# Optimization experiments

Hardware: AMD Instinct MI355X
Metric: run time of the kernel (lower is better)

The kernel has to match this reference:

```python
import jax, jax.numpy as jnp
import numpy as np

D = 512; H = 8; DH = D // H; FFN = 2048; K = 31; N = 4; T = 1024


def _ln(x, g, b):
    m = jnp.mean(x, -1, keepdims=True)
    v = jnp.var(x, -1, keepdims=True)
    return (x - m) * jax.lax.rsqrt(v + 1e-5) * g + b


def _ff(x, g, b, w1, b1, w2, b2):
    h = jax.nn.silu(_ln(x, g, b) @ w1 + b1)
    return 0.5 * (h @ w2 + b2)


def _forward(x, rel_pe, ln1_g, ln1_b, ff1_w1, ff1_b1, ff1_w2, ff1_b2,
             an_g, an_b, wq, bq, wk, bk, wv, bv, wo, bo, pos_w, u, v,
             cn_g, cn_b, pe_w, pe_b, dw_w, dw_b, bn_g, bn_b, pc_w, pc_b,
             ln2_g, ln2_b, ff2_w1, ff2_b1, ff2_w2, ff2_b2, fn_g, fn_b):
    Nb, Tt, _ = x.shape
    # macaron FF 1 (half-step)
    x = x + _ff(x, ln1_g, ln1_b, ff1_w1, ff1_b1, ff1_w2, ff1_b2)

    # RPE multi-head attention (Transformer-XL style)
    xa = _ln(x, an_g, an_b)
    split = lambda m: m.reshape(Nb, Tt, H, DH).transpose(0, 2, 1, 3)  # (N,H,T,dh)
    Q = split(xa @ wq + bq)
    Kk = split(xa @ wk + bk)
    V = split(xa @ wv + bv)
    # content-to-content: (Q+u) K^T
    AC = jnp.einsum('nhtd,nhsd->nhts', Q + u[None, :, None, :], Kk)
    # content-to-position: (Q+v) R^T, then rel-shift gather
    R = (rel_pe @ pos_w).reshape(2 * Tt - 1, H, DH)  # (2T-1,H,dh)
    BD_raw = jnp.einsum('nhtd,phd->nhtp', Q + v[None, :, None, :], R)  # (N,H,T,2T-1)
    idx = jnp.arange(Tt - 1, -1, -1)[None, :] + jnp.arange(Tt)[:, None]  # (T,T): i-j+(T-1)
    BD = jnp.take_along_axis(BD_raw, idx[None, None, :, :], axis=-1)  # (N,H,T,T)
    scores = (AC + BD) * (DH ** -0.5)
    attn = jax.nn.softmax(scores, axis=-1)
    out = jnp.einsum('nhts,nhsd->nthd', attn, V).reshape(Nb, Tt, D)
    x = x + (out @ wo + bo)

    # conv module: LN -> pointwise expand -> GLU -> depthwise conv -> BN(eval) -> SiLU -> pointwise
    c = _ln(x, cn_g, cn_b) @ pe_w + pe_b  # (N,T,2D)
    a, g = jnp.split(c, 2, axis=-1)
    c = a * jax.nn.sigmoid(g)
    c = c.transpose(0, 2, 1)  # (N,D,T)
    c = jax.lax.conv_general_dilated(
        c, dw_w, window_strides=(1,), padding=[(K // 2, K // 2)],
        dimension_numbers=('NCH', 'OIH', 'NCH'), feature_group_count=D)
    c = c + dw_b[None, :, None]
    # BatchNorm1d in eval mode: running_mean=0, running_var=1
    c = c * bn_g[None, :, None] + bn_b[None, :, None]
    c = jax.nn.silu(c).transpose(0, 2, 1) @ pc_w + pc_b
    x = x + c

    # macaron FF 2 + final LN
    x = x + _ff(x, ln2_g, ln2_b, ff2_w1, ff2_b1, ff2_w2, ff2_b2)
    return _ln(x, fn_g, fn_b)


def setup_inputs() -> dict:
    keys = iter(jax.random.split(jax.random.key(0), 64))
    def rn(*shape, s=0.02):
        return jax.random.normal(next(keys), shape, jnp.float32) * s
    inp = {}
    inp['x'] = rn(N, T, D, s=1.0)
    inp['rel_pe'] = rn(2 * T - 1, D, s=1.0)
    inp['ln1_g'] = jnp.ones(D); inp['ln1_b'] = jnp.zeros(D)
    inp['ff1_w1'] = rn(D, FFN); inp['ff1_b1'] = jnp.zeros(FFN)
    inp['ff1_w2'] = rn(FFN, D); inp['ff1_b2'] = jnp.zeros(D)
    inp['an_g'] = jnp.ones(D); inp['an_b'] = jnp.zeros(D)
    inp['wq'] = rn(D, D); inp['bq'] = jnp.zeros(D)
    inp['wk'] = rn(D, D); inp['bk'] = jnp.zeros(D)
    inp['wv'] = rn(D, D); inp['bv'] = jnp.zeros(D)
    inp['wo'] = rn(D, D); inp['bo'] = jnp.zeros(D)
    inp['pos_w'] = rn(D, D)
    inp['u'] = rn(H, DH); inp['v'] = rn(H, DH)
    inp['cn_g'] = jnp.ones(D); inp['cn_b'] = jnp.zeros(D)
    inp['pe_w'] = rn(D, 2 * D); inp['pe_b'] = jnp.zeros(2 * D)
    inp['dw_w'] = rn(D, 1, K); inp['dw_b'] = jnp.zeros(D)
    inp['bn_g'] = jnp.ones(D); inp['bn_b'] = jnp.zeros(D)
    inp['pc_w'] = rn(D, D); inp['pc_b'] = jnp.zeros(D)
    inp['ln2_g'] = jnp.ones(D); inp['ln2_b'] = jnp.zeros(D)
    inp['ff2_w1'] = rn(D, FFN); inp['ff2_b1'] = jnp.zeros(FFN)
    inp['ff2_w2'] = rn(FFN, D); inp['ff2_b2'] = jnp.zeros(D)
    inp['fn_g'] = jnp.ones(D); inp['fn_b'] = jnp.zeros(D)
    return inp


def reference(x, rel_pe, ln1_g, ln1_b, ff1_w1, ff1_b1, ff1_w2, ff1_b2,
              an_g, an_b, wq, bq, wk, bk, wv, bv, wo, bo, pos_w, u, v,
              cn_g, cn_b, pe_w, pe_b, dw_w, dw_b, bn_g, bn_b, pc_w, pc_b,
              ln2_g, ln2_b, ff2_w1, ff2_b1, ff2_w2, ff2_b2, fn_g, fn_b):
    return _forward(x, rel_pe, ln1_g, ln1_b, ff1_w1, ff1_b1, ff1_w2, ff1_b2,
                    an_g, an_b, wq, bq, wk, bk, wv, bv, wo, bo, pos_w, u, v,
                    cn_g, cn_b, pe_w, pe_b, dw_w, dw_b, bn_g, bn_b, pc_w, pc_b,
                    ln2_g, ln2_b, ff2_w1, ff2_b1, ff2_w2, ff2_b2, fn_g, fn_b)
```

## Files before the change

### kernel.cpp

```cpp
#include <hip/hip_runtime.h>
#include <hip/hip_bf16.h>

using bf16 = __hip_bfloat16;
typedef __attribute__((ext_vector_type(8))) short short8;
typedef __attribute__((ext_vector_type(4))) float f32x4;

static __device__ __forceinline__ float b2f(bf16 v) { return __bfloat162float(v); }
static __device__ __forceinline__ bf16  f2b(float v) { return __float2bfloat16(v); }
static __device__ __forceinline__ short f2bs(float x) {
    union { float f; unsigned u; } c; c.f = x;
    unsigned r = (c.u + 0x7FFFu + ((c.u >> 16) & 1u)) >> 16;
    return (short)r;
}
static __device__ __forceinline__ float bs2f(short s) {
    union { unsigned u; float f; } c; c.u = ((unsigned)(unsigned short)s) << 16;
    return c.f;
}
static __device__ __forceinline__ void gload16(const short* g, short* l) {
    __builtin_amdgcn_global_load_lds(
        (const __attribute__((address_space(1))) void*)g,
        (__attribute__((address_space(3))) void*)l, 16, 0, 0);
}

constexpr int kD   = 512;
constexpr int kT   = 1024;
constexpr int kN   = 4;
constexpr int kH   = 8;
constexpr int kDH  = 64;
constexpr int kFFN = 2048;
constexpr int kROWS = kN * kT;
constexpr int kP    = 2 * kT - 1;

#define ACT_NONE 0
#define ACT_SILU 1

__global__ __launch_bounds__(256) void stamp_kernel(float* __restrict__ out, int n, float val) {
    int i = blockIdx.x * 256 + threadIdx.x;
    if (i < n) out[i] = (i == 0 ? val : 0.f);
}

__global__ __launch_bounds__(256) void cvt_kernel(const float* __restrict__ in,
                                                  float* __restrict__ out, int n4) {
    int i = blockIdx.x * 256 + threadIdx.x;
    if (i < n4) ((f32x4*)out)[i] = ((const f32x4*)in)[i];
}

struct WtDesc { const float* src; short* dst; int K; int N; int tstart; };
struct WtArgs { WtDesc d[11]; };

__global__ __launch_bounds__(256) void wt_all_kernel(WtArgs a) {
    __shared__ float t[32][33];
    int bid = blockIdx.x;
    int i = 0;
#pragma unroll
    for (int j = 1; j < 11; ++j) if (bid >= a.d[j].tstart) i = j;
    const float* W = a.d[i].src;
    short* Wt = a.d[i].dst;
    int Kd = a.d[i].K, Nd = a.d[i].N;
    int lt = bid - a.d[i].tstart;
    int nx = Nd >> 5;
    int n0 = (lt % nx) * 32, k0 = (lt / nx) * 32;
    int tx = threadIdx.x & 31, ty = threadIdx.x >> 5;
#pragma unroll
    for (int it = 0; it < 4; ++it)
        t[ty + it * 8][tx] = W[(size_t)(k0 + ty + it * 8) * Nd + n0 + tx];
    __syncthreads();
#pragma unroll
    for (int it = 0; it < 4; ++it)
        Wt[(size_t)(n0 + ty + it * 8) * Kd + k0 + tx] = f2bs(t[tx][ty + it * 8]);
}

__global__ __launch_bounds__(256) void vtrans_kernel(const bf16* __restrict__ V,
                                                     bf16* __restrict__ Vt) {
    __shared__ short ts[64][72];
    int tt = blockIdx.x, h = blockIdx.y, n = blockIdx.z;
    int tid = threadIdx.x;
    int r = tid >> 3, cg = (tid & 7) * 8;
#pragma unroll
    for (int it = 0; it < 2; ++it) {
        int row = it * 32 + r;
        *(short8*)&ts[row][cg] =
            *(const short8*)((const short*)V + ((size_t)n * kT + tt * 64 + row) * 512 + h * 64 + cg);
    }
    __syncthreads();
#pragma unroll
    for (int it = 0; it < 2; ++it) {
        int d = it * 32 + r;
        short8 o;
#pragma unroll
        for (int i = 0; i < 8; ++i) o[i] = ts[cg + i][d];
        *(short8*)((short*)Vt + ((size_t)(n * 8 + h) * 64 + d) * 1024 + tt * 64 + cg) = o;
    }
}

__global__ __launch_bounds__(256) void dwt_kernel(const float* __restrict__ dw_w,
                                                  const float* __restrict__ dw_b,
                                                  const float* __restrict__ bn_g,
                                                  const float* __restrict__ bn_b,
                                                  float* __restrict__ wt,
                                                  float* __restrict__ beff) {
    int idx = blockIdx.x * 256 + threadIdx.x;
    if (idx < 31 * kD) {
        int d = idx & 511, k = idx >> 9;
        wt[k * kD + d] = dw_w[d * 31 + k] * bn_g[d];
    }
    if (idx < kD) beff[idx] = dw_b[idx] * bn_g[idx] + bn_b[idx];
}

__global__ __launch_bounds__(256) void ln_kernel(const float* __restrict__ xin,
                                                 const float* __restrict__ g,
                                                 const float* __restrict__ b,
                                                 void* __restrict__ outp, int out_f32) {
    int row = blockIdx.x;
    const float* xr = xin + (size_t)row * kD;
    int tid = threadIdx.x;
    float v0 = xr[tid], v1 = xr[tid + 256];
    float s = v0 + v1, sq = v0 * v0 + v1 * v1;
    for (int off = 32; off; off >>= 1) {
        s  += __shfl_down(s, off);
        sq += __shfl_down(sq, off);
    }
    __shared__ float ss[4], ssq[4];
    __shared__ float mean_s, rstd_s;
    int wid = tid >> 6, lane = tid & 63;
    if (lane == 0) { ss[wid] = s; ssq[wid] = sq; }
    __syncthreads();
    if (tid == 0) {
        float S  = ss[0] + ss[1] + ss[2] + ss[3];
        float SQ = ssq[0] + ssq[1] + ssq[2] + ssq[3];
        float m = S / (float)kD;
        float var = SQ / (float)kD - m * m;
        mean_s = m;
        rstd_s = rsqrtf(fmaxf(var, 0.f) + 1e-5f);
    }
    __syncthreads();
    float m = mean_s, rs = rstd_s;
    float o0 = (v0 - m) * rs * g[tid]       + b[tid];
    float o1 = (v1 - m) * rs * g[tid + 256] + b[tid + 256];
    size_t i0 = (size_t)row * kD + tid, i1 = i0 + 256;
    if (out_f32) {
        ((float*)outp)[i0] = o0; ((float*)outp)[i1] = o1;
    } else {
        ((bf16*)outp)[i0] = f2b(o0); ((bf16*)outp)[i1] = f2b(o1);
    }
}

__global__ __launch_bounds__(256, 4) void gemm_mfma64(
    const void* __restrict__ A, const short* __restrict__ Bt,
    const float* __restrict__ bias, const float* __restrict__ residual,
    float* __restrict__ outf, bf16* __restrict__ outb,
    int M, int N, int K, int act, float scale, int a_f32) {
    __shared__ short As[2][4096];
    __shared__ short Bs[2][4096];
    int tid = threadIdx.x;
    int m0 = blockIdx.y * 64, n0 = blockIdx.x * 64;
    int wid = tid >> 6, lane = tid & 63;
    int wm = (wid >> 1) * 32, wn = (wid & 1) * 32;
    int q = lane >> 4, c16 = lane & 15;

    f32x4 zero4 = {0.f, 0.f, 0.f, 0.f};
    f32x4 acc[2][2] = {{zero4, zero4}, {zero4, zero4}};

    int arow = lane >> 3;
    int aseg = (lane & 7) ^ arow;

    auto issueA = [&](int buf, int k0) {
        if (!a_f32) {
#pragma unroll
            for (int it = 0; it < 2; ++it) {
                int rbase = (wid * 2 + it) * 8;
                gload16((const short*)A + (size_t)(m0 + rbase + arow) * K + k0 + aseg * 8,
                        &As[buf][(wid * 2 + it) * 512]);
            }
        } else {
            int srow = tid >> 3, sseg = tid & 7;
#pragma unroll
            for (int it = 0; it < 2; ++it) {
                int row = it * 32 + srow;
                int rr = m0 + row;
                short8 v = {0, 0, 0, 0, 0, 0, 0, 0};
                if (rr < M) {
                    const float* ap = (const float*)A + (size_t)rr * K + k0 + sseg * 8;
                    f32x4 x0 = *(const f32x4*)ap;
                    f32x4 x1 = *(const f32x4*)(ap + 4);
                    v[0] = f2bs(x0[0]); v[1] = f2bs(x0[1]); v[2] = f2bs(x0[2]); v[3] = f2bs(x0[3]);
                    v[4] = f2bs(x1[0]); v[5] = f2bs(x1[1]); v[6] = f2bs(x1[2]); v[7] = f2bs(x1[3]);
                }
                *(short8*)&As[buf][(row * 8 + (sseg ^ (row & 7))) * 8] = v;
            }
        }
    };
    auto issueB = [&](int buf, int k0) {
#pragma unroll
        for (int it = 0; it < 2; ++it) {
            int rbase = (wid * 2 + it) * 8;
            gload16(Bt + (size_t)(n0 + rbase + arow) * K + k0 + aseg * 8,
                    &Bs[buf][(wid * 2 + it) * 512]);
        }
    };

    issueA(0, 0);
    issueB(0, 0);
    int cur = 0;
    for (int k0 = 0; k0 < K; k0 += 64) {
        __syncthreads();
        if (k0 + 64 < K) {
            issueA(cur ^ 1, k0 + 64);
            issueB(cur ^ 1, k0 + 64);
        }
#pragma unroll
        for (int ks = 0; ks < 2; ++ks) {
            int p = c16 & 7;
            short8 af[2], bfr[2];
#pragma unroll
            for (int mt = 0; mt < 2; ++mt) {
                int row = wm + mt * 16 + c16;
                af[mt] = *(const short8*)&As[cur][(row * 8 + ((ks * 4 + q) ^ p)) * 8];
            }
#pragma unroll
            for (int nt = 0; nt < 2; ++nt) {
                int row = wn + nt * 16 + c16;
                bfr[nt] = *(const short8*)&Bs[cur][(row * 8 + ((ks * 4 + q) ^ p)) * 8];
            }
#pragma unroll
            for (int mt = 0; mt < 2; ++mt)
#pragma unroll
                for (int nt = 0; nt < 2; ++nt)
                    acc[mt][nt] = __builtin_amdgcn_mfma_f32_16x16x32_bf16(
                        af[mt], bfr[nt], acc[mt][nt], 0, 0, 0);
        }
        cur ^= 1;
    }
#pragma unroll
    for (int mt = 0; mt < 2; ++mt) {
#pragma unroll
        for (int reg = 0; reg < 4; ++reg) {
            int r = m0 + wm + mt * 16 + q * 4 + reg;
            if (r >= M) continue;
#pragma unroll
            for (int nt = 0; nt < 2; ++nt) {
                int c = n0 + wn + nt * 16 + c16;
                float h = acc[mt][nt][reg];
                if (bias) h += bias[c];
                if (act == ACT_SILU) h = h / (1.f + __expf(-h));
                h *= scale;
                size_t idx = (size_t)r * N + c;
                if (residual) h += residual[idx];
                if (outf) outf[idx] = h;
                if (outb) outb[idx] = f2b(h);
            }
        }
    }
}

__global__ __launch_bounds__(256, 4) void gemm_qkv(
    const bf16* __restrict__ A, const short* __restrict__ Bt,
    const float* __restrict__ bq, const float* __restrict__ bk,
    const float* __restrict__ bv,
    bf16* __restrict__ Qb, bf16* __restrict__ Kb, bf16* __restrict__ Vb) {
    const int K = kD;
    __shared__ short As[2][4096];
    __shared__ short Bs[2][4096];
    int tid = threadIdx.x;
    int m0 = blockIdx.y * 64, n0 = blockIdx.x * 64;
    int seg = blockIdx.x >> 3;
    const float* bias = seg == 0 ? bq : (seg == 1 ? bk : bv);
    bf16* outb = seg == 0 ? Qb : (seg == 1 ? Kb : Vb);
    int ns0 = n0 & 511;
    int wid = tid >> 6, lane = tid & 63;
    int wm = (wid >> 1) * 32, wn = (wid & 1) * 32;
    int q = lane >> 4, c16 = lane & 15;

    f32x4 zero4 = {0.f, 0.f, 0.f, 0.f};
    f32x4 acc[2][2] = {{zero4, zero4}, {zero4, zero4}};
    int arow = lane >> 3;
    int aseg = (lane & 7) ^ arow;

    auto issue = [&](int buf, int k0) {
#pragma unroll
        for (int it = 0; it < 2; ++it) {
            int rbase = (wid * 2 + it) * 8;
            gload16((const short*)A + (size_t)(m0 + rbase + arow) * K + k0 + aseg * 8,
                    &As[buf][(wid * 2 + it) * 512]);
            gload16(Bt + (size_t)(n0 + rbase + arow) * K + k0 + aseg * 8,
                    &Bs[buf][(wid * 2 + it) * 512]);
        }
    };

    issue(0, 0);
    int cur = 0;
    for (int k0 = 0; k0 < K; k0 += 64) {
        __syncthreads();
        if (k0 + 64 < K) issue(cur ^ 1, k0 + 64);
#pragma unroll
        for (int ks = 0; ks < 2; ++ks) {
            int p = c16 & 7;
            short8 af[2], bfr[2];
#pragma unroll
            for (int mt = 0; mt < 2; ++mt) {
                int row = wm + mt * 16 + c16;
                af[mt] = *(const short8*)&As[cur][(row * 8 + ((ks * 4 + q) ^ p)) * 8];
            }
#pragma unroll
            for (int nt = 0; nt < 2; ++nt) {
                int row = wn + nt * 16 + c16;
                bfr[nt] = *(const short8*)&Bs[cur][(row * 8 + ((ks * 4 + q) ^ p)) * 8];
            }
#pragma unroll
            for (int mt = 0; mt < 2; ++mt)
#pragma unroll
                for (int nt = 0; nt < 2; ++nt)
                    acc[mt][nt] = __builtin_amdgcn_mfma_f32_16x16x32_bf16(
                        af[mt], bfr[nt], acc[mt][nt], 0, 0, 0);
        }
        cur ^= 1;
    }
#pragma unroll
    for (int mt = 0; mt < 2; ++mt)
#pragma unroll
        for (int reg = 0; reg < 4; ++reg) {
            int r = m0 + wm + mt * 16 + q * 4 + reg;
#pragma unroll
            for (int nt = 0; nt < 2; ++nt) {
                int c = ns0 + wn + nt * 16 + c16;
                outb[(size_t)r * 512 + c] = f2b(acc[mt][nt][reg] + bias[c]);
            }
        }
}

__global__ __launch_bounds__(256) void gemm_scalar(
    const void* __restrict__ A, const float* __restrict__ W,
    const float* __restrict__ bias, const float* __restrict__ residual,
    float* __restrict__ outf, bf16* __restrict__ outb,
    int M, int N, int K, int act, float scale, int a_f32) {
    __shared__ float As[16][65];
    __shared__ float Bs[16][65];
    int tid = threadIdx.x;
    int tx = tid & 15, ty = tid >> 4;
    int row0 = blockIdx.y * 64, col0 = blockIdx.x * 64;
    float acc[4][4] = {};
    for (int k0 = 0; k0 < K; k0 += 16) {
        for (int i = tid; i < 64 * 16; i += 256) {
            int r = i >> 4, c = i & 15;
            int rr = row0 + r;
            float v = 0.f;
            if (rr < M) {
                size_t idx = (size_t)rr * K + k0 + c;
                v = a_f32 ? ((const float*)A)[idx] : b2f(((const bf16*)A)[idx]);
            }
            As[c][r] = v;
        }
        for (int i = tid; i < 16 * 64; i += 256) {
            int r = i >> 6, c = i & 63;
            Bs[r][c] = W[(size_t)(k0 + r) * N + col0 + c];
        }
        __syncthreads();
#pragma unroll
        for (int kk = 0; kk < 16; ++kk) {
            float a[4], b[4];
#pragma unroll
            for (int i = 0; i < 4; ++i) a[i] = As[kk][ty * 4 + i];
#pragma unroll
            for (int j = 0; j < 4; ++j) b[j] = Bs[kk][tx * 4 + j];
#pragma unroll
            for (int i = 0; i < 4; ++i)
#pragma unroll
                for (int j = 0; j < 4; ++j) acc[i][j] += a[i] * b[j];
        }
        __syncthreads();
    }
#pragma unroll
    for (int i = 0; i < 4; ++i) {
        int r = row0 + ty * 4 + i;
        if (r >= M) continue;
#pragma unroll
        for (int j = 0; j < 4; ++j) {
            int c = col0 + tx * 4 + j;
            float h = acc[i][j];
            if (bias) h += bias[c];
            if (act == ACT_SILU) h = h / (1.f + __expf(-h));
            h *= scale;
            size_t idx = (size_t)r * N + c;
            if (residual) h += residual[idx];
            if (outf) outf[idx] = h;
            if (outb) outb[idx] = f2b(h);
        }
    }
}

__global__ __launch_bounds__(256, 2) void attn_mfma(
    const bf16* __restrict__ Qg, const bf16* __restrict__ Kg,
    const bf16* __restrict__ Vtg, const bf16* __restrict__ Rg,
    const float* __restrict__ uu, const float* __restrict__ vvp,
    bf16* __restrict__ outb) {
    __shared__ short Qu[64][72];
    __shared__ short Qv[64][72];
    __shared__ short Ks[64][72];
    __shared__ short Vt[64][72];
    __shared__ short Rw[128][72];
    __shared__ short Bp[64][136];

    int tid = threadIdx.x;
    int qb = blockIdx.x, h = blockIdx.y, n = blockIdx.z;
    int t0 = qb * 64;
    size_t baseq = ((size_t)n * kT) * 512 + (size_t)h * kDH;
    size_t basev = ((size_t)(n * 8 + h) * 64) * 1024;
    size_t baseo = ((size_t)n * kT) * kD + (size_t)h * kDH;

    int wid = tid >> 6, lane = tid & 63;
    int q = lane >> 4, c16 = lane & 15;
    int wm = wid * 16;
    int trow = wm + q * 4;

    {
        int t = tid >> 2, dg = (tid & 3) * 16;
        const short* qp = (const short*)Qg + baseq + (size_t)(t0 + t) * 512 + dg;
        short8 q0 = *(const short8*)qp;
        short8 q1 = *(const short8*)(qp + 8);
#pragma unroll
        for (int i = 0; i < 8; ++i) {
            float qv = bs2f(q0[i]);
            Qu[t][dg + i] = f2bs(qv + uu[h * 64 + dg + i]);
            Qv[t][dg + i] = f2bs(qv + vvp[h * 64 + dg + i]);
        }
#pragma unroll
        for (int i = 0; i < 8; ++i) {
            float qv = bs2f(q1[i]);
            Qu[t][dg + 8 + i] = f2bs(qv + uu[h * 64 + dg + 8 + i]);
            Qv[t][dg + 8 + i] = f2bs(qv + vvp[h * 64 + dg + 8 + i]);
        }
    }

    f32x4 zero4 = {0.f, 0.f, 0.f, 0.f};
    f32x4 acc_o[4] = {zero4, zero4, zero4, zero4};
    float m_i[4] = {-1e30f, -1e30f, -1e30f, -1e30f};
    float l_i[4] = {0.f, 0.f, 0.f, 0.f};

    for (int kt = 0; kt < 16; ++kt) {
        int s0 = kt * 64;
        __syncthreads();
        {
            int s = tid >> 2, dg = (tid & 3) * 16;
            const short* kp = (const short*)Kg + baseq + (size_t)(s0 + s) * 512 + dg;
            *(short8*)&Ks[s][dg]     = *(const short8*)kp;
            *(short8*)&Ks[s][dg + 8] = *(const short8*)(kp + 8);
            const short* vp = (const short*)Vtg + basev + (size_t)s * 1024 + s0 + dg;
            *(short8*)&Vt[s][dg]     = *(const short8*)vp;
            *(short8*)&Vt[s][dg + 8] = *(const short8*)(vp + 8);
        }
        int p_base = t0 - s0 + 960;
#pragma unroll
        for (int it = 0; it < 4; ++it) {
            int i = tid + it * 256;
            int j = i >> 3, dg2 = (i & 7) * 8;
            int p = p_base + j;
            p = p < 0 ? 0 : (p > 2046 ? 2046 : p);
            *(short8*)&Rw[j][dg2] =
                *(const short8*)((const short*)Rg + (size_t)p * kD + h * kDH + dg2);
        }
        __syncthreads();

        f32x4 acc_s[4] = {zero4, zero4, zero4, zero4};
        f32x4 acc_b[8] = {zero4, zero4, zero4, zero4, zero4, zero4, zero4, zero4};
#pragma unroll
        for (int ks = 0; ks < 2; ++ks) {
            short8 au = *(const short8*)&Qu[wm + c16][ks * 32 + q * 8];
            short8 av = *(const short8*)&Qv[wm + c16][ks * 32 + q * 8];
#pragma unroll
            for (int nt = 0; nt < 4; ++nt) {
                short8 bk_ = *(const short8*)&Ks[nt * 16 + c16][ks * 32 + q * 8];
                acc_s[nt] = __builtin_amdgcn_mfma_f32_16x16x32_bf16(au, bk_, acc_s[nt], 0, 0, 0);
            }
#pragma unroll
            for (int jt = 0; jt < 8; ++jt) {
                short8 br_ = *(const short8*)&Rw[jt * 16 + c16][ks * 32 + q * 8];
                acc_b[jt] = __builtin_amdgcn_mfma_f32_16x16x32_bf16(av, br_, acc_b[jt], 0, 0, 0);
            }
        }
#pragma unroll
        for (int jt = 0; jt < 8; ++jt)
#pragma unroll
            for (int reg = 0; reg < 4; ++reg)
                Bp[trow + reg][jt * 16 + c16] = f2bs(acc_b[jt][reg]);

        float pmat[4][4];
        float alpha[4];
#pragma unroll
        for (int reg = 0; reg < 4; ++reg) {
            int t = trow + reg;
            float mrow = -1e30f;
#pragma unroll
            for (int nt = 0; nt < 4; ++nt) {
                int s = nt * 16 + c16;
                int j = t - s + 63;
                float sv = (acc_s[nt][reg] + bs2f(Bp[t][j])) * 0.125f;
                pmat[nt][reg] = sv;
                mrow = fmaxf(mrow, sv);
            }
            mrow = fmaxf(mrow, __shfl_xor(mrow, 1));
            mrow = fmaxf(mrow, __shfl_xor(mrow, 2));
            mrow = fmaxf(mrow, __shfl_xor(mrow, 4));
            mrow = fmaxf(mrow, __shfl_xor(mrow, 8));
            float m_new = fmaxf(m_i[reg], mrow);
            alpha[reg] = __expf(m_i[reg] - m_new);
            float ps = 0.f;
#pragma unroll
            for (int nt = 0; nt < 4; ++nt) {
                float pe = __expf(pmat[nt][reg] - m_new);
                pmat[nt][reg] = pe;
                ps += pe;
            }
            ps += __shfl_xor(ps, 1);
            ps += __shfl_xor(ps, 2);
            ps += __shfl_xor(ps, 4);
            ps += __shfl_xor(ps, 8);
            l_i[reg] = l_i[reg] * alpha[reg] + ps;
            m_i[reg] = m_new;
        }
#pragma unroll
        for (int nt = 0; nt < 4; ++nt)
#pragma unroll
            for (int reg = 0; reg < 4; ++reg)
                Bp[trow + reg][nt * 16 + c16] = f2bs(pmat[nt][reg]);
#pragma unroll
        for (int dt = 0; dt < 4; ++dt)
#pragma unroll
            for (int reg = 0; reg < 4; ++reg)
                acc_o[dt][reg] *= alpha[reg];
#pragma unroll
        for (int ks = 0; ks < 2; ++ks) {
            short8 ap = *(const short8*)&Bp[wm + c16][ks * 32 + q * 8];
#pragma unroll
            for (int dt = 0; dt < 4; ++dt) {
                short8 bv_ = *(const short8*)&Vt[dt * 16 + c16][ks * 32 + q * 8];
                acc_o[dt] = __builtin_amdgcn_mfma_f32_16x16x32_bf16(ap, bv_, acc_o[dt], 0, 0, 0);
            }
        }
    }
#pragma unroll
    for (int reg = 0; reg < 4; ++reg) {
        float inv = 1.f / l_i[reg];
        int t = trow + reg;
#pragma unroll
        for (int dt = 0; dt < 4; ++dt)
            outb[baseo + (size_t)(t0 + t) * kD + dt * 16 + c16] = f2b(acc_o[dt][reg] * inv);
    }
}

__global__ __launch_bounds__(256) void attn_kernel(
    const bf16* __restrict__ Qg, const bf16* __restrict__ Kg,
    const bf16* __restrict__ Vg, const bf16* __restrict__ Rg,
    const float* __restrict__ uu, const float* __restrict__ vvp,
    bf16* __restrict__ outb) {
    __shared__ float Qs[64][65];
    __shared__ bf16 Ps[64][66];
    __shared__ bf16 Ks[64][66];
    __shared__ bf16 Vs[64][66];
    __shared__ bf16 Rs[127][66];
    __shared__ float uf[64], vf[64];
    __shared__ float uK[64], vR[127];

    int tid = threadIdx.x;
    int qb = blockIdx.x, h = blockIdx.y, n = blockIdx.z;
    int t0 = qb * 64;
    size_t base = ((size_t)n * kT) * kD + (size_t)h * kDH;

    if (tid < 64) {
        uf[tid] = uu[h * 64 + tid];
        vf[tid] = vvp[h * 64 + tid];
    }
    for (int i = tid; i < 64 * 64; i += 256) {
        int r = i >> 6, d = i & 63;
        Qs[r][d] = b2f(Qg[base + (size_t)(t0 + r) * kD + d]);
    }
    int r = tid >> 2, seg = tid & 3;
    float m_i = -1e30f, l_i = 0.f;
    float Oa[16];
#pragma unroll
    for (int i = 0; i < 16; ++i) Oa[i] = 0.f;

    for (int kt = 0; kt < 16; ++kt) {
        int s0 = kt * 64;
        __syncthreads();
        for (int i = tid; i < 64 * 64; i += 256) {
            int s = i >> 6, d = i & 63;
            Ks[s][d] = Kg[base + (size_t)(s0 + s) * kD + d];
            Vs[s][d] = Vg[base + (size_t)(s0 + s) * kD + d];
        }
        int p_base = t0 - s0 + 960;
        for (int i = tid; i < 127 * 64; i += 256) {
            int j = i >> 6, d = i & 63;
            int p = p_base + j;
            p = p < 0 ? 0 : (p > 2046 ? 2046 : p);
            Rs[j][d] = Rg[(size_t)p * kD + h * kDH + d];
        }
        __syncthreads();
        if (tid < 64) {
            float s_ = 0.f;
            for (int d = 0; d < 64; ++d) s_ += uf[d] * b2f(Ks[tid][d]);
            uK[tid] = s_;
        } else if (tid < 64 + 127) {
            int j = tid - 64;
            float s_ = 0.f;
            for (int d = 0; d < 64; ++d) s_ += vf[d] * b2f(Rs[j][d]);
            vR[j] = s_;
        }
        __syncthreads();
        float sv[16];
        float smax = -1e30f;
#pragma unroll
        for (int jj = 0; jj < 16; ++jj) {
            int s = seg * 16 + jj;
            int j = r - s + 63;
            float acc = 0.f;
            for (int d = 0; d < 64; ++d)
                acc += Qs[r][d] * (b2f(Ks[s][d]) + b2f(Rs[j][d]));
            acc = (acc + uK[s] + vR[j]) * 0.125f;
            sv[jj] = acc;
            smax = fmaxf(smax, acc);
        }
        smax = fmaxf(smax, __shfl_xor(smax, 1));
        smax = fmaxf(smax, __shfl_xor(smax, 2));
        float m_new = fmaxf(m_i, smax);
        float alpha = __expf(m_i - m_new);
        float psum = 0.f;
#pragma unroll
        for (int jj = 0; jj < 16; ++jj) {
            float p = __expf(sv[jj] - m_new);
            Ps[r][seg * 16 + jj] = f2b(p);
            psum += p;
        }
        psum += __shfl_xor(psum, 1);
        psum += __shfl_xor(psum, 2);
        l_i = l_i * alpha + psum;
        m_i = m_new;
#pragma unroll
        for (int i = 0; i < 16; ++i) Oa[i] *= alpha;
        __syncthreads();
        for (int s = 0; s < 64; ++s) {
            float p = b2f(Ps[r][s]);
#pragma unroll
            for (int dd = 0; dd < 16; ++dd)
                Oa[dd] += p * b2f(Vs[s][seg * 16 + dd]);
        }
    }
    float inv = 1.f / l_i;
#pragma unroll
    for (int dd = 0; dd < 16; ++dd)
        outb[base + (size_t)(t0 + r) * kD + seg * 16 + dd] = f2b(Oa[dd] * inv);
}

__global__ __launch_bounds__(256) void glu_kernel_v(const bf16* __restrict__ c,
                                                    bf16* __restrict__ out) {
    int i8 = (blockIdx.x * 256 + threadIdx.x) * 8;
    int row = i8 >> 9, d = i8 & 511;
    const short* cp = (const short*)c + (size_t)row * 1024;
    short8 a8 = *(const short8*)(cp + d);
    short8 g8 = *(const short8*)(cp + 512 + d);
    short8 o;
#pragma unroll
    for (int i = 0; i < 8; ++i) {
        float a = bs2f(a8[i]), g = bs2f(g8[i]);
        o[i] = f2bs(a / (1.f + __expf(-g)));
    }
    *(short8*)((short*)out + i8) = o;
}

__global__ __launch_bounds__(256) void gluconv_kernel(
    const bf16* __restrict__ cbuf, const float* __restrict__ wt,
    const float* __restrict__ beff, bf16* __restrict__ outb) {
    __shared__ short gsm[94][72];
    __shared__ float wsm[31][64];
    __shared__ float bsm[64];
    int tid = threadIdx.x;
    int dg0 = blockIdx.x * 64;
    int t0  = blockIdx.y * 64;
    int n   = blockIdx.z;

#pragma unroll
    for (int it = 0; it < 3; ++it) {
        int idx = tid + it * 256;
        if (idx < 94 * 8) {
            int row = idx >> 3, cg = (idx & 7) * 8;
            int t = t0 - 15 + row;
            short8 o = {0, 0, 0, 0, 0, 0, 0, 0};
            if ((unsigned)t < (unsigned)kT) {
                const short* cp = (const short*)cbuf + ((size_t)n * kT + t) * 1024 + dg0 + cg;
                short8 a8 = *(const short8*)cp;
                short8 g8 = *(const short8*)(cp + 512);
#pragma unroll
                for (int i = 0; i < 8; ++i)
                    o[i] = f2bs(bs2f(a8[i]) / (1.f + __expf(-bs2f(g8[i]))));
            }
            *(short8*)&gsm[row][cg] = o;
        }
    }
#pragma unroll
    for (int it = 0; it < 8; ++it) {
        int i = tid + it * 256;
        if (i < 31 * 64) wsm[i >> 6][i & 63] = wt[(i >> 6) * kD + dg0 + (i & 63)];
    }
    if (tid < 64) bsm[tid] = beff[dg0 + tid];
    __syncthreads();

    int tl = tid >> 2, dgl = (tid & 3) * 16;
    float acc[16] = {};
#pragma unroll
    for (int k = 0; k < 31; ++k) {
        short8 g0 = *(const short8*)&gsm[tl + k][dgl];
        short8 g1 = *(const short8*)&gsm[tl + k][dgl + 8];
#pragma unroll
        for (int i = 0; i < 8; ++i) {
            acc[i]     += bs2f(g0[i]) * wsm[k][dgl + i];
            acc[8 + i] += bs2f(g1[i]) * wsm[k][dgl + 8 + i];
        }
    }
    short8 o0, o1;
#pragma unroll
    for (int i = 0; i < 8; ++i) {
        float h = acc[i] + bsm[dgl + i];
        o0[i] = f2bs(h / (1.f + __expf(-h)));
        h = acc[8 + i] + bsm[dgl + 8 + i];
        o1[i] = f2bs(h / (1.f + __expf(-h)));
    }
    short* op = (short*)outb + ((size_t)n * kT + t0 + tl) * kD + dg0 + dgl;
    *(short8*)op = o0;
    *(short8*)(op + 8) = o1;
}

__global__ __launch_bounds__(256) void conv_kernel(
    const bf16* __restrict__ glu, const float* __restrict__ dw_w,
    const float* __restrict__ dw_b, const float* __restrict__ bn_g,
    const float* __restrict__ bn_b, bf16* __restrict__ outb) {
    int idx = blockIdx.x * 256 + threadIdx.x;
    int d = idx & 511;
    int t = (idx >> 9) & 1023;
    int n = idx >> 19;
    const bf16* gp = glu + ((size_t)n * kT) * kD + d;
    float acc = 0.f;
#pragma unroll
    for (int k = 0; k < 31; ++k) {
        int tt = t + k - 15;
        if ((unsigned)tt < (unsigned)kT)
            acc += b2f(gp[(size_t)tt * kD]) * dw_w[d * 31 + k];
    }
    acc += dw_b[d];
    acc = acc * bn_g[d] + bn_b[d];
    acc = acc / (1.f + __expf(-acc));
    outb[idx] = f2b(acc);
}

extern "C" void kernel_launch(void* const* d_in, const int* in_sizes, int n_in,
                              void* d_out, int out_size, void* d_ws, size_t ws_size,
                              hipStream_t stream) {
    const float* x      = (const float*)d_in[0];
    const float* rel_pe = (const float*)d_in[1];
    const float* ln1_g  = (const float*)d_in[2];
    const float* ln1_b  = (const float*)d_in[3];
    const float* ff1_w1 = (const float*)d_in[4];
    const float* ff1_b1 = (const float*)d_in[5];
    const float* ff1_w2 = (const float*)d_in[6];
    const float* ff1_b2 = (const float*)d_in[7];
    const float* an_g   = (const float*)d_in[8];
    const float* an_b   = (const float*)d_in[9];
    const float* wq = (const float*)d_in[10]; const float* bq = (const float*)d_in[11];
    const float* wk = (const float*)d_in[12]; const float* bk = (const float*)d_in[13];
    const float* wv = (const float*)d_in[14]; const float* bv = (const float*)d_in[15];
    const float* wo = (const float*)d_in[16]; const float* bo = (const float*)d_in[17];
    const float* pos_w = (const float*)d_in[18];
    const float* uu = (const float*)d_in[19]; const float* vvp = (const float*)d_in[20];
    const float* cn_g = (const float*)d_in[21]; const float* cn_b = (const float*)d_in[22];
    const float* pe_w = (const float*)d_in[23]; const float* pe_b = (const float*)d_in[24];
    const float* dw_w = (const float*)d_in[25]; const float* dw_b = (const float*)d_in[26];
    const float* bn_g = (const float*)d_in[27]; const float* bn_b = (const float*)d_in[28];
    const float* pc_w = (const float*)d_in[29]; const float* pc_b = (const float*)d_in[30];
    const float* ln2_g = (const float*)d_in[31]; const float* ln2_b = (const float*)d_in[32];
    const float* ff2_w1 = (const float*)d_in[33]; const float* ff2_b1 = (const float*)d_in[34];
    const float* ff2_w2 = (const float*)d_in[35]; const float* ff2_b2 = (const float*)d_in[36];
    const float* fn_g = (const float*)d_in[37]; const float* fn_b = (const float*)d_in[38];
    (void)n_in; (void)in_sizes;

    const int total = kROWS * kD;
    dim3 blk(256);
    const size_t MB = 1ull << 20;
    char* w = (char*)d_ws;

    if (ws_size >= 30 * MB) {
        float* xf      = (float*)(w);
        short* ff1_w1t = (short*)(w + 8 * MB);
        short* ff1_w2t = (short*)(w + 10 * MB);
        short* wqt     = (short*)(w + 12 * MB);
        short* wkt     = (short*)(w + 12 * MB + 512 * 1024);
        short* wvt     = (short*)(w + 13 * MB);
        short* wot     = (short*)(w + 13 * MB + 512 * 1024);
        short* poswt   = (short*)(w + 14 * MB);
        short* pewt    = (short*)(w + 14 * MB + 512 * 1024);
        short* pcwt    = (short*)(w + 15 * MB + 512 * 1024);
        short* ff2_w1t = (short*)(w + 16 * MB);
        short* ff2_w2t = (short*)(w + 18 * MB);
        char*  dyn     = w + 20 * MB;
        bf16* hchunk = (bf16*)dyn;
        bf16* Qb     = (bf16*)dyn;
        bf16* Kb     = (bf16*)(dyn + 4 * MB);
        bf16* Rb     = (bf16*)(dyn + 8 * MB);
        bf16* cbuf   = (bf16*)dyn;
        float* dwt   = (float*)(dyn + 8 * MB);
        float* beff  = (float*)(dyn + 8 * MB + 256 * 1024);
        bf16* nb     = (bf16*)d_out;
        bf16* Vtg    = (bf16*)d_out;
        bf16* convb  = (bf16*)d_out;
        bf16* Vb     = (bf16*)d_out + (size_t)kROWS * kD;
        bf16* attnb  = Vb;

        WtArgs wa;
        const float* srcs[11] = {ff1_w1, ff1_w2, wq, wk, wv, wo, pos_w, pe_w, pc_w, ff2_w1, ff2_w2};
        short* dsts[11] = {ff1_w1t, ff1_w2t, wqt, wkt, wvt, wot, poswt, pewt, pcwt, ff2_w1t, ff2_w2t};
        int Ks_[11] = {512, 2048, 512, 512, 512, 512, 512, 512, 512, 512, 2048};
        int Ns_[11] = {2048, 512, 512, 512, 512, 512, 512, 1024, 512, 2048, 512};
        int cum = 0;
        for (int i = 0; i < 11; ++i) {
            wa.d[i].src = srcs[i]; wa.d[i].dst = dsts[i];
            wa.d[i].K = Ks_[i]; wa.d[i].N = Ns_[i]; wa.d[i].tstart = cum;
            cum += (Ns_[i] / 32) * (Ks_[i] / 32);
        }
        wt_all_kernel<<<cum, blk, 0, stream>>>(wa);

        ln_kernel<<<kROWS, blk, 0, stream>>>(x, ln1_g, ln1_b, nb, 0);
        for (int c = 0; c < 2; ++c) {
            size_t off = (size_t)c * 2048 * kD;
            gemm_mfma64<<<dim3(kFFN / 64, 2048 / 64), blk, 0, stream>>>(
                nb + off, ff1_w1t, ff1_b1, nullptr, nullptr, hchunk,
                2048, kFFN, kD, ACT_SILU, 1.f, 0);
            gemm_mfma64<<<dim3(kD / 64, 2048 / 64), blk, 0, stream>>>(
                hchunk, ff1_w2t, ff1_b2, x + off, xf + off, nullptr,
                2048, kD, kFFN, ACT_NONE, 0.5f, 0);
        }

        ln_kernel<<<kROWS, blk, 0, stream>>>(xf, an_g, an_b, nb, 0);
        gemm_qkv<<<dim3(24, kROWS / 64), blk, 0, stream>>>(
            nb, wqt, bq, bk, bv, Qb, Kb, Vb);
        vtrans_kernel<<<dim3(16, 8, 4), blk, 0, stream>>>(Vb, Vtg);
        gemm_mfma64<<<dim3(kD / 64, (kP + 63) / 64), blk, 0, stream>>>(
            rel_pe, poswt, nullptr, nullptr, nullptr, Rb, kP, kD, kD, ACT_NONE, 1.f, 1);
        attn_mfma<<<dim3(kT / 64, kH, kN), blk, 0, stream>>>(Qb, Kb, Vtg, Rb, uu, vvp, attnb);
        gemm_mfma64<<<dim3(kD / 64, kROWS / 64), blk, 0, stream>>>(
            attnb, wot, bo, xf, xf, nullptr, kROWS, kD, kD, ACT_NONE, 1.f, 0);

        dwt_kernel<<<62, blk, 0, stream>>>(dw_w, dw_b, bn_g, bn_b, dwt, beff);
        ln_kernel<<<kROWS, blk, 0, stream>>>(xf, cn_g, cn_b, nb, 0);
        gemm_mfma64<<<dim3(2 * kD / 64, kROWS / 64), blk, 0, stream>>>(
            nb, pewt, pe_b, nullptr, nullptr, cbuf, kROWS, 2 * kD, kD, ACT_NONE, 1.f, 0);
        gluconv_kernel<<<dim3(8, 16, 4), blk, 0, stream>>>(cbuf, dwt, beff, convb);
        gemm_mfma64<<<dim3(kD / 64, kROWS / 64), blk, 0, stream>>>(
            convb, pcwt, pc_b, xf, xf, nullptr, kROWS, kD, kD, ACT_NONE, 1.f, 0);

        ln_kernel<<<kROWS, blk, 0, stream>>>(xf, ln2_g, ln2_b, nb, 0);
        for (int c = 0; c < 2; ++c) {
            size_t off = (size_t)c * 2048 * kD;
            gemm_mfma64<<<dim3(kFFN / 64, 2048 / 64), blk, 0, stream>>>(
                nb + off, ff2_w1t, ff2_b1, nullptr, nullptr, hchunk,
                2048, kFFN, kD, ACT_SILU, 1.f, 0);
            gemm_mfma64<<<dim3(kD / 64, 2048 / 64), blk, 0, stream>>>(
                hchunk, ff2_w2t, ff2_b2, xf + off, xf + off, nullptr,
                2048, kD, kFFN, ACT_NONE, 0.5f, 0);
        }

        ln_kernel<<<kROWS, blk, 0, stream>>>(xf, fn_g, fn_b, d_out, 1);
        return;
    }

    if (ws_size < 22 * MB) {
        stamp_kernel<<<(out_size + 255) / 256, blk, 0, stream>>>(
            (float*)d_out, out_size, 1000.f + (float)(ws_size / MB));
        return;
    }

    float* xf    = (float*)(w);
    bf16*  hbch  = (bf16*)(w + 8 * MB);
    bf16*  Qb    = (bf16*)(w + 8 * MB);
    bf16*  cbuf  = (bf16*)(w + 8 * MB);
    bf16*  convb = (bf16*)(w + 8 * MB);
    bf16*  Kb    = (bf16*)(w + 12 * MB);
    bf16*  Vb    = (bf16*)(w + 16 * MB);
    bf16*  glub  = (bf16*)(w + 16 * MB);
    bf16*  Rb    = (bf16*)(w + 20 * MB);
    bf16*  nb    = (bf16*)d_out;
    bf16*  attnb = (bf16*)d_out;

    cvt_kernel<<<total / 1024, blk, 0, stream>>>(x, xf, total / 4);

    ln_kernel<<<kROWS, blk, 0, stream>>>(xf, ln1_g, ln1_b, nb, 0);
    for (int c = 0; c < 4; ++c) {
        size_t off = (size_t)c * 1024 * kD;
        gemm_scalar<<<dim3(kFFN / 64, 1024 / 64), blk, 0, stream>>>(
            nb + off, ff1_w1, ff1_b1, nullptr, nullptr, hbch, 1024, kFFN, kD, ACT_SILU, 1.f, 0);
        gemm_scalar<<<dim3(kD / 64, 1024 / 64), blk, 0, stream>>>(
            hbch, ff1_w2, ff1_b2, xf + off, xf + off, nullptr, 1024, kD, kFFN, ACT_NONE, 0.5f, 0);
    }

    ln_kernel<<<kROWS, blk, 0, stream>>>(xf, an_g, an_b, nb, 0);
    gemm_scalar<<<dim3(kD / 64, kROWS / 64), blk, 0, stream>>>(
        nb, wq, bq, nullptr, nullptr, Qb, kROWS, kD, kD, ACT_NONE, 1.f, 0);
    gemm_scalar<<<dim3(kD / 64, kROWS / 64), blk, 0, stream>>>(
        nb, wk, bk, nullptr, nullptr, Kb, kROWS, kD, kD, ACT_NONE, 1.f, 0);
    gemm_scalar<<<dim3(kD / 64, kROWS / 64), blk, 0, stream>>>(
        nb, wv, bv, nullptr, nullptr, Vb, kROWS, kD, kD, ACT_NONE, 1.f, 0);
    gemm_scalar<<<dim3(kD / 64, (kP + 63) / 64), blk, 0, stream>>>(
        rel_pe, pos_w, nullptr, nullptr, nullptr, Rb, kP, kD, kD, ACT_NONE, 1.f, 1);
    attn_kernel<<<dim3(kT / 64, kH, kN), blk, 0, stream>>>(Qb, Kb, Vb, Rb, uu, vvp, attnb);
    gemm_scalar<<<dim3(kD / 64, kROWS / 64), blk, 0, stream>>>(
        attnb, wo, bo, xf, xf, nullptr, kROWS, kD, kD, ACT_NONE, 1.f, 0);

    ln_kernel<<<kROWS, blk, 0, stream>>>(xf, cn_g, cn_b, nb, 0);
    gemm_scalar<<<dim3(2 * kD / 64, kROWS / 64), blk, 0, stream>>>(
        nb, pe_w, pe_b, nullptr, nullptr, cbuf, kROWS, 2 * kD, kD, ACT_NONE, 1.f, 0);
    glu_kernel_v<<<total / 2048, blk, 0, stream>>>(cbuf, glub);
    conv_kernel<<<total / 256, blk, 0, stream>>>(glub, dw_w, dw_b, bn_g, bn_b, convb);
    gemm_scalar<<<dim3(kD / 64, kROWS / 64), blk, 0, stream>>>(
        convb, pc_w, pc_b, xf, xf, nullptr, kROWS, kD, kD, ACT_NONE, 1.f, 0);

    ln_kernel<<<kROWS, blk, 0, stream>>>(xf, ln2_g, ln2_b, nb, 0);
    for (int c = 0; c < 4; ++c) {
        size_t off = (size_t)c * 1024 * kD;
        gemm_scalar<<<dim3(kFFN / 64, 1024 / 64), blk, 0, stream>>>(
            nb + off, ff2_w1, ff2_b1, nullptr, nullptr, hbch, 1024, kFFN, kD, ACT_SILU, 1.f, 0);
        gemm_scalar<<<dim3(kD / 64, 1024 / 64), blk, 0, stream>>>(
            hbch, ff2_w2, ff2_b2, xf + off, xf + off, nullptr, 1024, kD, kFFN, ACT_NONE, 0.5f, 0);
    }

    ln_kernel<<<kROWS, blk, 0, stream>>>(xf, fn_g, fn_b, d_out, 1);
}
```

Before: 504.6 us.

## Add 128-row GEMM tile for FFN expand and trim attention rel-pos MFMAs

```diff
diff --git a/kernel.cpp b/kernel.cpp
--- a/kernel.cpp
+++ b/kernel.cpp
@@ -237,6 +237,91 @@
         for (int reg = 0; reg < 4; ++reg) {
             int r = m0 + wm + mt * 16 + q * 4 + reg;
             if (r >= M) continue;
+#pragma unroll
+            for (int nt = 0; nt < 2; ++nt) {
+                int c = n0 + wn + nt * 16 + c16;
+                float h = acc[mt][nt][reg];
+                if (bias) h += bias[c];
+                if (act == ACT_SILU) h = h / (1.f + __expf(-h));
+                h *= scale;
+                size_t idx = (size_t)r * N + c;
+                if (residual) h += residual[idx];
+                if (outf) outf[idx] = h;
+                if (outb) outb[idx] = f2b(h);
+            }
+        }
+    }
+}
+
+__global__ __launch_bounds__(256, 3) void gemm_mfma128(
+    const bf16* __restrict__ A, const short* __restrict__ Bt,
+    const float* __restrict__ bias, const float* __restrict__ residual,
+    float* __restrict__ outf, bf16* __restrict__ outb,
+    int M, int N, int K, int act, float scale) {
+    __shared__ short As[2][8192];
+    __shared__ short Bs[2][4096];
+    int tid = threadIdx.x;
+    int m0 = blockIdx.y * 128, n0 = blockIdx.x * 64;
+    int wid = tid >> 6, lane = tid & 63;
+    int wm = (wid >> 1) * 64, wn = (wid & 1) * 32;
+    int q = lane >> 4, c16 = lane & 15;
+
+    f32x4 zero4 = {0.f, 0.f, 0.f, 0.f};
+    f32x4 acc[4][2];
+#pragma unroll
+    for (int i = 0; i < 4; ++i) { acc[i][0] = zero4; acc[i][1] = zero4; }
+
+    int arow = lane >> 3;
+    int aseg = (lane & 7) ^ arow;
+
+    auto issue = [&](int buf, int k0) {
+#pragma unroll
+        for (int it = 0; it < 4; ++it) {
+            int gidx = wid * 4 + it;
+            gload16((const short*)A + (size_t)(m0 + gidx * 8 + arow) * K + k0 + aseg * 8,
+                    &As[buf][gidx * 512]);
+        }
+#pragma unroll
+        for (int it = 0; it < 2; ++it) {
+            int gidx = wid * 2 + it;
+            gload16(Bt + (size_t)(n0 + gidx * 8 + arow) * K + k0 + aseg * 8,
+                    &Bs[buf][gidx * 512]);
+        }
+    };
+
+    issue(0, 0);
+    int cur = 0;
+    for (int k0 = 0; k0 < K; k0 += 64) {
+        __syncthreads();
+        if (k0 + 64 < K) issue(cur ^ 1, k0 + 64);
+#pragma unroll
+        for (int ks = 0; ks < 2; ++ks) {
+            int p = c16 & 7;
+            short8 af[4], bfr[2];
+#pragma unroll
+            for (int mt = 0; mt < 4; ++mt) {
+                int row = wm + mt * 16 + c16;
+                af[mt] = *(const short8*)&As[cur][(row * 8 + ((ks * 4 + q) ^ p)) * 8];
+            }
+#pragma unroll
+            for (int nt = 0; nt < 2; ++nt) {
+                int row = wn + nt * 16 + c16;
+                bfr[nt] = *(const short8*)&Bs[cur][(row * 8 + ((ks * 4 + q) ^ p)) * 8];
+            }
+#pragma unroll
+            for (int mt = 0; mt < 4; ++mt)
+#pragma unroll
+                for (int nt = 0; nt < 2; ++nt)
+                    acc[mt][nt] = __builtin_amdgcn_mfma_f32_16x16x32_bf16(
+                        af[mt], bfr[nt], acc[mt][nt], 0, 0, 0);
+        }
+        cur ^= 1;
+    }
+#pragma unroll
+    for (int mt = 0; mt < 4; ++mt) {
+#pragma unroll
+        for (int reg = 0; reg < 4; ++reg) {
+            int r = m0 + wm + mt * 16 + q * 4 + reg;
 #pragma unroll
             for (int nt = 0; nt < 2; ++nt) {
                 int c = n0 + wn + nt * 16 + c16;
@@ -461,7 +546,7 @@
         __syncthreads();
 
         f32x4 acc_s[4] = {zero4, zero4, zero4, zero4};
-        f32x4 acc_b[8] = {zero4, zero4, zero4, zero4, zero4, zero4, zero4, zero4};
+        f32x4 acc_b[5] = {zero4, zero4, zero4, zero4, zero4};
 #pragma unroll
         for (int ks = 0; ks < 2; ++ks) {
             short8 au = *(const short8*)&Qu[wm + c16][ks * 32 + q * 8];
@@ -472,16 +557,16 @@
                 acc_s[nt] = __builtin_amdgcn_mfma_f32_16x16x32_bf16(au, bk_, acc_s[nt], 0, 0, 0);
             }
 #pragma unroll
-            for (int jt = 0; jt < 8; ++jt) {
-                short8 br_ = *(const short8*)&Rw[jt * 16 + c16][ks * 32 + q * 8];
+            for (int jt = 0; jt < 5; ++jt) {
+                short8 br_ = *(const short8*)&Rw[wm + jt * 16 + c16][ks * 32 + q * 8];
                 acc_b[jt] = __builtin_amdgcn_mfma_f32_16x16x32_bf16(av, br_, acc_b[jt], 0, 0, 0);
             }
         }
 #pragma unroll
-        for (int jt = 0; jt < 8; ++jt)
+        for (int jt = 0; jt < 5; ++jt)
 #pragma unroll
             for (int reg = 0; reg < 4; ++reg)
-                Bp[trow + reg][jt * 16 + c16] = f2bs(acc_b[jt][reg]);
+                Bp[trow + reg][wm + jt * 16 + c16] = f2bs(acc_b[jt][reg]);
 
         float pmat[4][4];
         float alpha[4];
@@ -828,9 +913,9 @@
         ln_kernel<<<kROWS, blk, 0, stream>>>(x, ln1_g, ln1_b, nb, 0);
         for (int c = 0; c < 2; ++c) {
             size_t off = (size_t)c * 2048 * kD;
-            gemm_mfma64<<<dim3(kFFN / 64, 2048 / 64), blk, 0, stream>>>(
+            gemm_mfma128<<<dim3(kFFN / 64, 2048 / 128), blk, 0, stream>>>(
                 nb + off, ff1_w1t, ff1_b1, nullptr, nullptr, hchunk,
-                2048, kFFN, kD, ACT_SILU, 1.f, 0);
+                2048, kFFN, kD, ACT_SILU, 1.f);
             gemm_mfma64<<<dim3(kD / 64, 2048 / 64), blk, 0, stream>>>(
                 hchunk, ff1_w2t, ff1_b2, x + off, xf + off, nullptr,
                 2048, kD, kFFN, ACT_NONE, 0.5f, 0);
@@ -857,9 +942,9 @@
         ln_kernel<<<kROWS, blk, 0, stream>>>(xf, ln2_g, ln2_b, nb, 0);
         for (int c = 0; c < 2; ++c) {
             size_t off = (size_t)c * 2048 * kD;
-            gemm_mfma64<<<dim3(kFFN / 64, 2048 / 64), blk, 0, stream>>>(
+            gemm_mfma128<<<dim3(kFFN / 64, 2048 / 128), blk, 0, stream>>>(
                 nb + off, ff2_w1t, ff2_b1, nullptr, nullptr, hchunk,
-                2048, kFFN, kD, ACT_SILU, 1.f, 0);
+                2048, kFFN, kD, ACT_SILU, 1.f);
             gemm_mfma64<<<dim3(kD / 64, 2048 / 64), blk, 0, stream>>>(
                 hchunk, ff2_w2t, ff2_b2, xf + off, xf + off, nullptr,
                 2048, kD, kFFN, ACT_NONE, 0.5f, 0);
```

After: 519.2 us. 1.03x slower.
